# Performance work log

Measured on AMD Instinct MI355X. Metric: run time of the kernel, lower is better.

## Reference

```python
import jax, jax.numpy as jnp
import numpy as np

D_MODEL = 1024
N_HEADS = 16
HEAD_DIM = D_MODEL // N_HEADS
SEQ_LEN = 2048
BATCH = 4


def setup_inputs() -> dict:
    key = jax.random.key(0)
    k1, k2, k3 = jax.random.split(key, 3)
    x = jax.random.normal(k1, (BATCH, SEQ_LEN, D_MODEL), dtype=jnp.float32)
    # Linear weights stored as [in, out] so y = x @ W (equivalent to torch x @ W.T)
    w_qkv = jax.random.normal(k2, (D_MODEL, 3 * D_MODEL), dtype=jnp.float32) * (D_MODEL ** -0.5)
    w_proj = jax.random.normal(k3, (D_MODEL, D_MODEL), dtype=jnp.float32) * (D_MODEL ** -0.5)
    return {"x": x, "w_qkv": w_qkv, "w_proj": w_proj}


def reference(x, w_qkv, w_proj):
    B, T, C = x.shape
    qkv = x @ w_qkv  # [B, T, 3C]
    q, k, v = jnp.split(qkv, 3, axis=-1)
    # [B, H, T, hd]
    q = q.reshape(B, T, N_HEADS, HEAD_DIM).transpose(0, 2, 1, 3)
    k = k.reshape(B, T, N_HEADS, HEAD_DIM).transpose(0, 2, 1, 3)
    v = v.reshape(B, T, N_HEADS, HEAD_DIM).transpose(0, 2, 1, 3)
    scale = HEAD_DIM ** -0.5
    attn = jnp.einsum("bhqd,bhkd->bhqk", q, k) * scale  # [B, H, T, T]
    causal = jnp.tril(jnp.ones((T, T), dtype=bool))
    attn = jnp.where(causal, attn, -jnp.inf)
    attn = jax.nn.softmax(attn, axis=-1)
    out = jnp.einsum("bhqk,bhkd->bhqd", attn, v)  # [B, H, T, hd]
    out = out.transpose(0, 2, 1, 3).reshape(B, T, C)
    return out @ w_proj
```

## Files before the change

### kernel.cpp

```cpp
#include <hip/hip_runtime.h>
#include <stdint.h>


typedef __bf16 bf16x8 __attribute__((ext_vector_type(8)));
typedef float f32x4 __attribute__((ext_vector_type(4)));
typedef unsigned short u16x8 __attribute__((ext_vector_type(8)));

#define DEVINL static __device__ __forceinline__

DEVINL unsigned short f2b(float f) {
  __bf16 h = (__bf16)f;
  return __builtin_bit_cast(unsigned short, h);
}

DEVINL void gld16(const void* g, void* l) {
  __builtin_amdgcn_global_load_lds(
      (const __attribute__((address_space(1))) void*)g,
      (__attribute__((address_space(3))) void*)l, 16, 0, 0);
}

DEVINL f32x4 mfma16(bf16x8 a, bf16x8 b, f32x4 c) {
  return __builtin_amdgcn_mfma_f32_16x16x32_bf16(a, b, c, 0, 0, 0);
}

#define SCHED_FENCE() __builtin_amdgcn_sched_barrier(0)

__global__ __launch_bounds__(256) void k_cast_bf16(const float* __restrict__ in,
                                                   unsigned short* __restrict__ out,
                                                   int n8) {
  int i = blockIdx.x * 256 + threadIdx.x;
  if (i >= n8) return;
  const float4* p = (const float4*)in + (size_t)i * 2;
  float4 a = p[0], b = p[1];
  u16x8 o;
  o[0] = f2b(a.x); o[1] = f2b(a.y); o[2] = f2b(a.z); o[3] = f2b(a.w);
  o[4] = f2b(b.x); o[5] = f2b(b.y); o[6] = f2b(b.z); o[7] = f2b(b.w);
  *(u16x8*)(out + (size_t)i * 8) = o;
}

__global__ __launch_bounds__(256) void k_transpose_w(const float* __restrict__ in,
                                                     unsigned short* __restrict__ out,
                                                     int R, int C) {
  __shared__ float t[64][65];
  int ci = blockIdx.x * 64, ri = blockIdx.y * 64;
  int tid = threadIdx.x;
#pragma unroll
  for (int j = 0; j < 4; ++j) {
    int c = tid + j * 256;
    int row = c >> 4;
    int col = (c & 15) * 4;
    float4 v = *(const float4*)(in + (size_t)(ri + row) * C + ci + col);
    t[row][col] = v.x; t[row][col + 1] = v.y; t[row][col + 2] = v.z; t[row][col + 3] = v.w;
  }
  __syncthreads();
  int cc = tid >> 2;
  int seg = (tid & 3) * 16;
  u16x8 o0, o1;
#pragma unroll
  for (int j = 0; j < 8; ++j) o0[j] = f2b(t[seg + j][cc]);
#pragma unroll
  for (int j = 0; j < 8; ++j) o1[j] = f2b(t[seg + 8 + j][cc]);
  unsigned short* dst = out + (size_t)(ci + cc) * R + ri + seg;
  *(u16x8*)dst = o0;
  *(u16x8*)(dst + 8) = o1;
}

template <int MODE>
__global__ __launch_bounds__(256) void k_gemm(const unsigned short* __restrict__ A,
                                              const unsigned short* __restrict__ Bt,
                                              int M, int N, int K,
                                              float* __restrict__ Cf,
                                              unsigned short* __restrict__ qo,
                                              unsigned short* __restrict__ ko,
                                              unsigned short* __restrict__ vo,
                                              float qscale) {
  __shared__ unsigned short As[2][128 * 32];
  __shared__ unsigned short Bs[2][128 * 32];
  int tid = threadIdx.x;
  int w = tid >> 6, lane = tid & 63, l15 = lane & 15, l4 = lane >> 4;
  int nwg = gridDim.x;
  int gy = M >> 7;
  int lin = blockIdx.x;
  int nx = nwg >> 3, rr = nwg & 7;
  int xcd = lin & 7, idx = lin >> 3;
  int wgid = (xcd < rr ? xcd * (nx + 1) : rr * (nx + 1) + (xcd - rr) * nx) + idx;
  int bn = wgid / gy, bm = wgid % gy;
  int wr = (w >> 1) * 64, wc = (w & 1) * 64;
  f32x4 acc[4][4];
#pragma unroll
  for (int i = 0; i < 4; ++i)
#pragma unroll
    for (int j = 0; j < 4; ++j) acc[i][j] = (f32x4){0.f, 0.f, 0.f, 0.f};
  const char* Ab = (const char*)(A + (size_t)bm * 128 * K);
  const char* Bb = (const char*)(Bt + (size_t)bn * 128 * K);
  int c_0 = tid, c_1 = tid + 256;
  int row0 = c_0 >> 2, cb0 = (c_0 & 3) * 16;
  int row1 = c_1 >> 2, cb1 = (c_1 & 3) * 16;

  auto stage = [&](int kt, int buf) {
    gld16(Ab + ((size_t)row0 * K + kt) * 2 + cb0, (char*)As[buf] + c_0 * 16);
    gld16(Bb + ((size_t)row0 * K + kt) * 2 + cb0, (char*)Bs[buf] + c_0 * 16);
    gld16(Ab + ((size_t)row1 * K + kt) * 2 + cb1, (char*)As[buf] + c_1 * 16);
    gld16(Bb + ((size_t)row1 * K + kt) * 2 + cb1, (char*)Bs[buf] + c_1 * 16);
  };

  const int nkt = K >> 5;
  stage(0, 0);
  SCHED_FENCE();
  for (int t = 0; t < nkt; ++t) {
    int cur = t & 1;
    if (t) {
      SCHED_FENCE();
      __builtin_amdgcn_s_barrier();
      SCHED_FENCE();
    }
    if (t + 1 < nkt) {
      stage((t + 1) * 32, cur ^ 1);
      SCHED_FENCE();
      asm volatile("s_waitcnt vmcnt(4)" ::: "memory");
    } else {
      SCHED_FENCE();
      asm volatile("s_waitcnt vmcnt(0)" ::: "memory");
    }
    SCHED_FENCE();
    __builtin_amdgcn_s_barrier();
    SCHED_FENCE();
    const char* Ac = (const char*)As[cur];
    const char* Bc = (const char*)Bs[cur];
    bf16x8 af[4], bfr[4];
#pragma unroll
    for (int m = 0; m < 4; ++m)
      af[m] = *(const bf16x8*)(Ac + (wr + m * 16 + l15) * 64 + l4 * 16);
#pragma unroll
    for (int n = 0; n < 4; ++n)
      bfr[n] = *(const bf16x8*)(Bc + (wc + n * 16 + l15) * 64 + l4 * 16);
    __builtin_amdgcn_s_setprio(1);
#pragma unroll
    for (int m = 0; m < 4; ++m)
#pragma unroll
      for (int n = 0; n < 4; ++n)
        acc[m][n] = mfma16(af[m], bfr[n], acc[m][n]);
    __builtin_amdgcn_s_setprio(0);
  }
#pragma unroll
  for (int m = 0; m < 4; ++m) {
    int grow0 = bm * 128 + wr + m * 16 + l4 * 4;
#pragma unroll
    for (int n = 0; n < 4; ++n) {
      int gcol = bn * 128 + wc + n * 16 + l15;
      if (MODE == 1) {
#pragma unroll
        for (int r = 0; r < 4; ++r)
          Cf[(size_t)(grow0 + r) * N + gcol] = acc[m][n][r];
      } else {
        int which = gcol >> 10, rem = gcol & 1023;
        int h = rem >> 6, d = rem & 63;
        int b = grow0 >> 11, t0 = grow0 & 2047;
        if (which == 2) {
          uint32_t lo = (uint32_t)f2b(acc[m][n][0]) | ((uint32_t)f2b(acc[m][n][1]) << 16);
          uint32_t hi = (uint32_t)f2b(acc[m][n][2]) | ((uint32_t)f2b(acc[m][n][3]) << 16);
          size_t off = (((size_t)(b * 16 + h)) * 64 + d) * 2048 + t0;
          *(uint2*)(vo + off) = make_uint2(lo, hi);
        } else {
          size_t off = (((size_t)(b * 16 + h)) * 2048 + t0) * 64 + d;
#pragma unroll
          for (int r = 0; r < 4; ++r) {
            float val = acc[m][n][r];
            if (which == 0) qo[off + (size_t)r * 64] = f2b(val * qscale);
            else            ko[off + (size_t)r * 64] = f2b(val);
          }
        }
      }
    }
  }
}

__global__ __launch_bounds__(512) void k_attn(const unsigned short* __restrict__ Q,
                                              const unsigned short* __restrict__ Kt,
                                              const unsigned short* __restrict__ Vt,
                                              unsigned short* __restrict__ AO) {
  __shared__ unsigned short Ks[2][4096];
  __shared__ unsigned short Vs[2][4096];
  __shared__ unsigned short Ps[8192];
  int tid = threadIdx.x;
  int w = tid >> 6, lane = tid & 63, l15 = lane & 15, l4 = lane >> 4;
  int lin = blockIdx.x;
  int xcd = lin & 7, jj = lin >> 3;
  int bh = xcd * 8 + (jj & 7);
  int p = jj >> 3;
  const char* Kb = (const char*)(Kt + (size_t)bh * 2048 * 64);
  const char* Vb = (const char*)(Vt + (size_t)bh * 64 * 2048);
  const int swp = (l15 & 7) << 4;
  char* Pw = (char*)Ps + w * 2048;
  int b = bh >> 4, h = bh & 15;

  int Lb0 = tid * 16;
  int Nb0 = Lb0 ^ (((Lb0 >> 7) & 7) << 4);
  int d0 = Nb0 >> 7, in0 = Nb0 & 127;

  auto stage = [&](int t, int buf) {
    size_t kv0 = (size_t)t * 64;
    gld16(Kb + kv0 * 128 + Nb0, (char*)Ks[buf] + Lb0);
    gld16(Vb + (size_t)d0 * 4096 + kv0 * 2 + in0, (char*)Vs[buf] + Lb0);
  };

  auto run = [&](int qi) {
    int q0 = qi * 128;
    const unsigned short* Qb = Q + ((size_t)bh * 2048 + q0 + w * 16) * 64;
    bf16x8 qf0 = *(const bf16x8*)((const char*)Qb + l15 * 128 + l4 * 16);
    bf16x8 qf1 = *(const bf16x8*)((const char*)Qb + l15 * 128 + 64 + l4 * 16);
    f32x4 o[4];
#pragma unroll
    for (int i = 0; i < 4; ++i) o[i] = (f32x4){0.f, 0.f, 0.f, 0.f};
    float mrow = -1e30f, lrow = 0.f;
    const int ntiles = 2 * qi + 2;
    const int qgmin = q0 + w * 16;
    const int qg = qgmin + l15;
    SCHED_FENCE();
    __builtin_amdgcn_s_barrier();
    SCHED_FENCE();
    stage(0, 0);
    SCHED_FENCE();
    for (int it = 0; it < ntiles; ++it) {
      int cur = it & 1;
      if (it) {
        SCHED_FENCE();
        __builtin_amdgcn_s_barrier();
        SCHED_FENCE();
      }
      if (it + 1 < ntiles) {
        stage(it + 1, cur ^ 1);
        SCHED_FENCE();
        asm volatile("s_waitcnt vmcnt(2)" ::: "memory");
      } else {
        SCHED_FENCE();
        asm volatile("s_waitcnt vmcnt(0)" ::: "memory");
      }
      SCHED_FENCE();
      __builtin_amdgcn_s_barrier();
      SCHED_FENCE();
      if (it * 64 <= qgmin + 15) {
        const char* Kc = (const char*)Ks[cur];
        const char* Vc = (const char*)Vs[cur];
        f32x4 s[4];
        __builtin_amdgcn_s_setprio(1);
#pragma unroll
        for (int c = 0; c < 4; ++c) {
          int row = c * 16 + l15;
          int base = row * 128 + l4 * 16;
          int sw = (row & 7) << 4;
          bf16x8 k0 = *(const bf16x8*)(Kc + (base ^ sw));
          bf16x8 k1 = *(const bf16x8*)(Kc + ((base + 64) ^ sw));
          f32x4 t = mfma16(k0, qf0, (f32x4){0.f, 0.f, 0.f, 0.f});
          s[c] = mfma16(k1, qf1, t);
        }
        __builtin_amdgcn_s_setprio(0);
        if (it * 64 + 63 > qgmin) {
#pragma unroll
          for (int c = 0; c < 4; ++c) {
            int kvb = it * 64 + c * 16 + l4 * 4;
#pragma unroll
            for (int r = 0; r < 4; ++r)
              if (kvb + r > qg) s[c][r] = -1e30f;
          }
        }
        float mx = fmaxf(fmaxf(fmaxf(s[0][0], s[0][1]), fmaxf(s[0][2], s[0][3])),
                         fmaxf(fmaxf(s[1][0], s[1][1]), fmaxf(s[1][2], s[1][3])));
        mx = fmaxf(mx, fmaxf(fmaxf(fmaxf(s[2][0], s[2][1]), fmaxf(s[2][2], s[2][3])),
                             fmaxf(fmaxf(s[3][0], s[3][1]), fmaxf(s[3][2], s[3][3]))));
        mx = fmaxf(mx, __shfl_xor(mx, 16));
        mx = fmaxf(mx, __shfl_xor(mx, 32));
        float mn = fmaxf(mrow, mx);
        float corr = __builtin_amdgcn_exp2f(mrow - mn);
        mrow = mn;
        float rs = 0.f;
#pragma unroll
        for (int c = 0; c < 4; ++c) {
          float p0 = __builtin_amdgcn_exp2f(s[c][0] - mn);
          float p1 = __builtin_amdgcn_exp2f(s[c][1] - mn);
          float p2 = __builtin_amdgcn_exp2f(s[c][2] - mn);
          float p3 = __builtin_amdgcn_exp2f(s[c][3] - mn);
          rs += (p0 + p1) + (p2 + p3);
          uint32_t lo = (uint32_t)f2b(p0) | ((uint32_t)f2b(p1) << 16);
          uint32_t hi = (uint32_t)f2b(p2) | ((uint32_t)f2b(p3) << 16);
          *(uint2*)(Pw + ((l15 * 128 + c * 32 + l4 * 8) ^ swp)) = make_uint2(lo, hi);
        }
        rs += __shfl_xor(rs, 16);
        rs += __shfl_xor(rs, 32);
        lrow = lrow * corr + rs;
        float corr_r[4];
#pragma unroll
        for (int r = 0; r < 4; ++r) corr_r[r] = __shfl(corr, l4 * 4 + r);
#pragma unroll
        for (int dc = 0; dc < 4; ++dc)
#pragma unroll
          for (int r = 0; r < 4; ++r) o[dc][r] *= corr_r[r];
        bf16x8 pa[2];
#pragma unroll
        for (int kc = 0; kc < 2; ++kc)
          pa[kc] = *(const bf16x8*)(Pw + ((l15 * 128 + kc * 64 + l4 * 16) ^ swp));
        __builtin_amdgcn_s_setprio(1);
#pragma unroll
        for (int dc = 0; dc < 4; ++dc) {
#pragma unroll
          for (int kc = 0; kc < 2; ++kc) {
            int vrow = dc * 16 + l15;
            int vnat = vrow * 128 + kc * 64 + l4 * 16;
            bf16x8 vb = *(const bf16x8*)(Vc + (vnat ^ ((vrow & 7) << 4)));
            o[dc] = mfma16(pa[kc], vb, o[dc]);
          }
        }
        __builtin_amdgcn_s_setprio(0);
      }
    }
    float inv[4];
#pragma unroll
    for (int r = 0; r < 4; ++r) inv[r] = 1.f / __shfl(lrow, l4 * 4 + r);
#pragma unroll
    for (int dc = 0; dc < 4; ++dc) {
#pragma unroll
      for (int r = 0; r < 4; ++r) {
        int t = q0 + w * 16 + l4 * 4 + r;
        AO[((size_t)(b * 2048 + t)) * 1024 + h * 64 + dc * 16 + l15] =
            f2b(o[dc][r] * inv[r]);
      }
    }
  };

  run(15 - p);
  run(p);
}

extern "C" void kernel_launch(void* const* d_in, const int* in_sizes, int n_in,
                              void* d_out, int out_size, void* d_ws, size_t ws_size,
                              hipStream_t stream) {
  const float* x      = (const float*)d_in[0];
  const float* w_qkv  = (const float*)d_in[1];
  const float* w_proj = (const float*)d_in[2];
  float* out = (float*)d_out;
  char* ws = (char*)d_ws;
  const size_t MB = 1024 * 1024;
  unsigned short* xb     = (unsigned short*)(ws);
  unsigned short* ao     = (unsigned short*)(ws);
  unsigned short* wqkvT  = (unsigned short*)(ws + 16 * MB);
  unsigned short* wprojT = (unsigned short*)(ws + 22 * MB);
  unsigned short* q      = (unsigned short*)(ws + 24 * MB);
  unsigned short* k      = (unsigned short*)(ws + 40 * MB);
  unsigned short* vT     = (unsigned short*)(ws + 56 * MB);

  k_cast_bf16<<<4096, 256, 0, stream>>>(x, xb, 1048576);
  k_transpose_w<<<dim3(48, 16), 256, 0, stream>>>(w_qkv, wqkvT, 1024, 3072);
  k_transpose_w<<<dim3(16, 16), 256, 0, stream>>>(w_proj, wprojT, 1024, 1024);
  const float qscale = 0.125f * 1.44269504088896f;
  k_gemm<0><<<1536, 256, 0, stream>>>(xb, wqkvT, 8192, 3072, 1024,
                                      nullptr, q, k, vT, qscale);
  k_attn<<<512, 512, 0, stream>>>(q, k, vT, ao);
  k_gemm<1><<<512, 256, 0, stream>>>(ao, wprojT, 8192, 1024, 1024,
                                     out, nullptr, nullptr, nullptr, 1.f);
}
```

Measured before the change: 190.7 us.

## Triple-buffer GEMM LDS staging, swizzle LDS layout, and reorder tile mapping

The GEMM kernel moves from double to triple buffering of its LDS tiles, prefetching two k-steps ahead and waiting with vmcnt(8) so more global loads are in flight while MFMAs run. It also applies an XOR swizzle to LDS addresses on both the global_load_lds writes and the fragment reads, to cut LDS bank conflicts. Workgroup-to-tile mapping becomes row-major over N tiles instead of column-major over M tiles, which changes L2 reuse per XCD. LDS use rises from 32KB to 48KB per block, which may reduce occupancy.

New measurement: 183.1 us. 4.0% less time.

```diff
diff --git a/kernel.cpp b/kernel.cpp
--- a/kernel.cpp
+++ b/kernel.cpp
@@ -74,17 +74,17 @@
                                               unsigned short* __restrict__ ko,
                                               unsigned short* __restrict__ vo,
                                               float qscale) {
-  __shared__ unsigned short As[2][128 * 32];
-  __shared__ unsigned short Bs[2][128 * 32];
+  __shared__ unsigned short As[3][128 * 32];
+  __shared__ unsigned short Bs[3][128 * 32];
   int tid = threadIdx.x;
   int w = tid >> 6, lane = tid & 63, l15 = lane & 15, l4 = lane >> 4;
   int nwg = gridDim.x;
-  int gy = M >> 7;
+  int gx = N >> 7;
   int lin = blockIdx.x;
   int nx = nwg >> 3, rr = nwg & 7;
   int xcd = lin & 7, idx = lin >> 3;
   int wgid = (xcd < rr ? xcd * (nx + 1) : rr * (nx + 1) + (xcd - rr) * nx) + idx;
-  int bn = wgid / gy, bm = wgid % gy;
+  int bn = wgid % gx, bm = wgid / gx;
   int wr = (w >> 1) * 64, wc = (w & 1) * 64;
   f32x4 acc[4][4];
 #pragma unroll
@@ -93,29 +93,36 @@
     for (int j = 0; j < 4; ++j) acc[i][j] = (f32x4){0.f, 0.f, 0.f, 0.f};
   const char* Ab = (const char*)(A + (size_t)bm * 128 * K);
   const char* Bb = (const char*)(Bt + (size_t)bn * 128 * K);
-  int c_0 = tid, c_1 = tid + 256;
-  int row0 = c_0 >> 2, cb0 = (c_0 & 3) * 16;
-  int row1 = c_1 >> 2, cb1 = (c_1 & 3) * 16;
+  int Lb0 = tid * 16, Lb1 = (tid + 256) * 16;
+  int Nb0 = Lb0 ^ (((Lb0 >> 7) & 3) << 4);
+  int Nb1 = Lb1 ^ (((Lb1 >> 7) & 3) << 4);
+  int rA0 = Nb0 >> 6, o0 = Nb0 & 63;
+  int rA1 = Nb1 >> 6, o1 = Nb1 & 63;
 
   auto stage = [&](int kt, int buf) {
-    gld16(Ab + ((size_t)row0 * K + kt) * 2 + cb0, (char*)As[buf] + c_0 * 16);
-    gld16(Bb + ((size_t)row0 * K + kt) * 2 + cb0, (char*)Bs[buf] + c_0 * 16);
-    gld16(Ab + ((size_t)row1 * K + kt) * 2 + cb1, (char*)As[buf] + c_1 * 16);
-    gld16(Bb + ((size_t)row1 * K + kt) * 2 + cb1, (char*)Bs[buf] + c_1 * 16);
+    gld16(Ab + ((size_t)rA0 * K + kt) * 2 + o0, (char*)As[buf] + Lb0);
+    gld16(Bb + ((size_t)rA0 * K + kt) * 2 + o0, (char*)Bs[buf] + Lb0);
+    gld16(Ab + ((size_t)rA1 * K + kt) * 2 + o1, (char*)As[buf] + Lb1);
+    gld16(Bb + ((size_t)rA1 * K + kt) * 2 + o1, (char*)Bs[buf] + Lb1);
   };
 
   const int nkt = K >> 5;
   stage(0, 0);
+  stage(32, 1);
   SCHED_FENCE();
   for (int t = 0; t < nkt; ++t) {
-    int cur = t & 1;
+    int cur = t - (t / 3) * 3;
     if (t) {
       SCHED_FENCE();
       __builtin_amdgcn_s_barrier();
       SCHED_FENCE();
     }
-    if (t + 1 < nkt) {
-      stage((t + 1) * 32, cur ^ 1);
+    if (t + 2 < nkt) {
+      int nb = (t + 2) - ((t + 2) / 3) * 3;
+      stage((t + 2) * 32, nb);
+      SCHED_FENCE();
+      asm volatile("s_waitcnt vmcnt(8)" ::: "memory");
+    } else if (t + 1 < nkt) {
       SCHED_FENCE();
       asm volatile("s_waitcnt vmcnt(4)" ::: "memory");
     } else {
@@ -129,11 +136,15 @@
     const char* Bc = (const char*)Bs[cur];
     bf16x8 af[4], bfr[4];
 #pragma unroll
-    for (int m = 0; m < 4; ++m)
-      af[m] = *(const bf16x8*)(Ac + (wr + m * 16 + l15) * 64 + l4 * 16);
-#pragma unroll
-    for (int n = 0; n < 4; ++n)
-      bfr[n] = *(const bf16x8*)(Bc + (wc + n * 16 + l15) * 64 + l4 * 16);
+    for (int m = 0; m < 4; ++m) {
+      int nat = (wr + m * 16 + l15) * 64 + l4 * 16;
+      af[m] = *(const bf16x8*)(Ac + (nat ^ (((nat >> 7) & 3) << 4)));
+    }
+#pragma unroll
+    for (int n = 0; n < 4; ++n) {
+      int nat = (wc + n * 16 + l15) * 64 + l4 * 16;
+      bfr[n] = *(const bf16x8*)(Bc + (nat ^ (((nat >> 7) & 3) << 4)));
+    }
     __builtin_amdgcn_s_setprio(1);
 #pragma unroll
     for (int m = 0; m < 4; ++m)
```
